# Kernel optimization log

Measured on AMD Instinct MI355X. Metric: run time of the kernel, lower is better.

The kernel has to match this reference:

```python
import jax, jax.numpy as jnp
import numpy as np

TAU = 1.0


def setup_inputs() -> dict:
    key = jax.random.key(0)
    k1, k2 = jax.random.split(key)
    z = jax.random.normal(k1, (131072, 64), dtype=jnp.float32)
    cluster_centers = jax.random.normal(k2, (512, 64), dtype=jnp.float32)
    return {"z": z, "cluster_centers": cluster_centers}


def reference(z, cluster_centers):
    # ||z - c||^2 = ||z||^2 + ||c||^2 - 2 z.c  (avoids the [B,K,D] broadcast tensor)
    z_sq = jnp.sum(z * z, axis=1, keepdims=True)              # [B, 1]
    c_sq = jnp.sum(cluster_centers * cluster_centers, axis=1)  # [K]
    cross = jnp.einsum('bd,kd->bk', z, cluster_centers)        # [B, K]
    dist_sq = z_sq + c_sq[None, :] - 2.0 * cross               # [B, K]
    q = jax.nn.softmax(-dist_sq / TAU, axis=1)                 # [B, K]
    loss = jnp.mean(jnp.sum(q * dist_sq, axis=1))
    return (q, loss)
```

## Files before the change

### kernel.cpp

```cpp
#include <hip/hip_runtime.h>

typedef short bf16x8 __attribute__((ext_vector_type(8)));
typedef float f32x4 __attribute__((ext_vector_type(4)));

#define K_CLUSTERS 512
#define DIM 64

__device__ __forceinline__ unsigned short f32_to_bf16_rne(float f) {
    unsigned int u = __float_as_uint(f);
    u += 0x7fffu + ((u >> 16) & 1u);
    return (unsigned short)(u >> 16);
}
__device__ __forceinline__ float bf16_bits_to_f32(unsigned short h) {
    return __uint_as_float(((unsigned int)h) << 16);
}

__global__ void prep_centers(const float* __restrict__ c,
                             short* __restrict__ c_hi, short* __restrict__ c_lo,
                             float* __restrict__ c_sq) {
    int idx = blockIdx.x * 256 + threadIdx.x;
    float v = c[idx];
    unsigned short h = f32_to_bf16_rne(v);
    float hf = bf16_bits_to_f32(h);
    unsigned short l = f32_to_bf16_rne(v - hf);
    c_hi[idx] = (short)h;
    c_lo[idx] = (short)l;
    float s = v * v;
    #pragma unroll
    for (int off = 1; off < 64; off <<= 1) s += __shfl_xor(s, off, 64);
    if ((threadIdx.x & 63) == 0) c_sq[idx >> 6] = s;
}

__global__ __launch_bounds__(256, 2)
void cluster_kernel(const float* __restrict__ z,
                    const short* __restrict__ c_hi,
                    const short* __restrict__ c_lo,
                    const float* __restrict__ c_sq,
                    float* __restrict__ q_out,
                    float* __restrict__ partials) {
    __shared__ __align__(16) short a_hi_s[16][72];
    __shared__ __align__(16) short a_lo_s[16][72];
    __shared__ float zsq_s[16];
    __shared__ float dist_s[16][K_CLUSTERS + 4];
    __shared__ float wloss_s[4];

    const int tid  = threadIdx.x;
    const int lane = tid & 63;
    const int wave = tid >> 6;
    const int m    = lane & 15;
    const int qd   = lane >> 4;
    const long rb  = (long)blockIdx.x * 16;

    bf16x8 bh[8][2], bl[8][2];
    #pragma unroll
    for (int t = 0; t < 8; ++t) {
        const int col = wave * 128 + t * 16 + m;
        const long boff = (long)col * DIM + qd * 8;
        #pragma unroll
        for (int kg = 0; kg < 2; ++kg) {
            bh[t][kg] = *(const bf16x8*)(c_hi + boff + kg * 32);
            bl[t][kg] = *(const bf16x8*)(c_lo + boff + kg * 32);
        }
    }

    {
        float4 v = ((const float4*)(z + rb * DIM))[tid];
        const int srow = tid >> 4;
        const int scol = (tid & 15) * 4;
        float fv[4] = {v.x, v.y, v.z, v.w};
        #pragma unroll
        for (int j = 0; j < 4; ++j) {
            unsigned short h = f32_to_bf16_rne(fv[j]);
            float hf = bf16_bits_to_f32(h);
            unsigned short l = f32_to_bf16_rne(fv[j] - hf);
            a_hi_s[srow][scol + j] = (short)h;
            a_lo_s[srow][scol + j] = (short)l;
        }
        float s = fv[0]*fv[0] + fv[1]*fv[1] + fv[2]*fv[2] + fv[3]*fv[3];
        #pragma unroll
        for (int off = 1; off < 16; off <<= 1) s += __shfl_xor(s, off, 64);
        if ((tid & 15) == 0) zsq_s[srow] = s;
    }
    __syncthreads();

    bf16x8 ah[2], al[2];
    #pragma unroll
    for (int kg = 0; kg < 2; ++kg) {
        ah[kg] = *(const bf16x8*)&a_hi_s[m][kg * 32 + qd * 8];
        al[kg] = *(const bf16x8*)&a_lo_s[m][kg * 32 + qd * 8];
    }

    f32x4 acc[8];
    #pragma unroll
    for (int t = 0; t < 8; ++t) acc[t] = (f32x4){0.f, 0.f, 0.f, 0.f};
    #pragma unroll
    for (int kg = 0; kg < 2; ++kg) {
        #pragma unroll
        for (int t = 0; t < 8; ++t) {
            acc[t] = __builtin_amdgcn_mfma_f32_16x16x32_bf16(ah[kg], bh[t][kg], acc[t], 0, 0, 0);
            acc[t] = __builtin_amdgcn_mfma_f32_16x16x32_bf16(ah[kg], bl[t][kg], acc[t], 0, 0, 0);
            acc[t] = __builtin_amdgcn_mfma_f32_16x16x32_bf16(al[kg], bh[t][kg], acc[t], 0, 0, 0);
        }
    }

    #pragma unroll
    for (int t = 0; t < 8; ++t) {
        const int col = wave * 128 + t * 16 + m;
        const float csq = c_sq[col];
        #pragma unroll
        for (int r = 0; r < 4; ++r) {
            const int row = qd * 4 + r;
            dist_s[row][col] = zsq_s[row] + csq - 2.0f * acc[t][r];
        }
    }
    __syncthreads();

    float lsum = 0.0f;
    #pragma unroll
    for (int rr = 0; rr < 4; ++rr) {
        const int row = wave * 4 + rr;
        float d[8];
        #pragma unroll
        for (int j = 0; j < 8; ++j) d[j] = dist_s[row][lane + 64 * j];
        float mn = d[0];
        #pragma unroll
        for (int j = 1; j < 8; ++j) mn = fminf(mn, d[j]);
        #pragma unroll
        for (int off = 1; off < 64; off <<= 1) mn = fminf(mn, __shfl_xor(mn, off, 64));
        float e[8], s = 0.0f;
        #pragma unroll
        for (int j = 0; j < 8; ++j) { e[j] = __expf(mn - d[j]); s += e[j]; }
        #pragma unroll
        for (int off = 1; off < 64; off <<= 1) s += __shfl_xor(s, off, 64);
        const float inv = 1.0f / s;
        float rl = 0.0f;
        float* orow = q_out + (rb + row) * K_CLUSTERS;
        #pragma unroll
        for (int j = 0; j < 8; ++j) {
            const float qv = e[j] * inv;
            orow[lane + 64 * j] = qv;
            rl += qv * d[j];
        }
        #pragma unroll
        for (int off = 1; off < 64; off <<= 1) rl += __shfl_xor(rl, off, 64);
        lsum += rl;
    }
    if (lane == 0) wloss_s[wave] = lsum;
    __syncthreads();
    if (tid == 0) partials[blockIdx.x] = wloss_s[0] + wloss_s[1] + wloss_s[2] + wloss_s[3];
}

__global__ void reduce_loss(const float* __restrict__ partials, int n,
                            float* __restrict__ loss_out, float inv_b) {
    float s = 0.f;
    for (int i = threadIdx.x; i < n; i += 256) s += partials[i];
    #pragma unroll
    for (int off = 1; off < 64; off <<= 1) s += __shfl_xor(s, off, 64);
    __shared__ float ws[4];
    if ((threadIdx.x & 63) == 0) ws[threadIdx.x >> 6] = s;
    __syncthreads();
    if (threadIdx.x == 0) loss_out[0] = (ws[0] + ws[1] + ws[2] + ws[3]) * inv_b;
}

extern "C" void kernel_launch(void* const* d_in, const int* in_sizes, int n_in,
                              void* d_out, int out_size, void* d_ws, size_t ws_size,
                              hipStream_t stream) {
    const float* z = (const float*)d_in[0];
    const float* c = (const float*)d_in[1];
    const int B = in_sizes[0] / DIM;
    float* q_out = (float*)d_out;
    float* loss_out = q_out + (size_t)B * K_CLUSTERS;

    char* ws = (char*)d_ws;
    short* c_hi    = (short*)ws;
    short* c_lo    = (short*)(ws + 65536);
    float* c_sq    = (float*)(ws + 131072);
    float* partials = (float*)(ws + 133120);

    const int nblk = B / 16;
    prep_centers<<<(K_CLUSTERS * DIM) / 256, 256, 0, stream>>>(c, c_hi, c_lo, c_sq);
    cluster_kernel<<<nblk, 256, 0, stream>>>(z, c_hi, c_lo, c_sq, q_out, partials);
    reduce_loss<<<1, 256, 0, stream>>>(partials, nblk, loss_out, 1.0f / (float)B);
}
```

Baseline: 395.7 us.

## Process four row tiles per block to reuse center fragments; atomic loss reduction

```diff
diff --git a/kernel.cpp b/kernel.cpp
--- a/kernel.cpp
+++ b/kernel.cpp
@@ -5,6 +5,7 @@
 
 #define K_CLUSTERS 512
 #define DIM 64
+#define ROWS_PER_BLOCK 64
 
 __device__ __forceinline__ unsigned short f32_to_bf16_rne(float f) {
     unsigned int u = __float_as_uint(f);
@@ -31,13 +32,18 @@
     if ((threadIdx.x & 63) == 0) c_sq[idx >> 6] = s;
 }
 
+__global__ void init_loss(float* __restrict__ loss_out) {
+    if (threadIdx.x == 0) loss_out[0] = 0.0f;
+}
+
 __global__ __launch_bounds__(256, 2)
 void cluster_kernel(const float* __restrict__ z,
                     const short* __restrict__ c_hi,
                     const short* __restrict__ c_lo,
                     const float* __restrict__ c_sq,
                     float* __restrict__ q_out,
-                    float* __restrict__ partials) {
+                    float* __restrict__ loss_out,
+                    float inv_b) {
     __shared__ __align__(16) short a_hi_s[16][72];
     __shared__ __align__(16) short a_lo_s[16][72];
     __shared__ float zsq_s[16];
@@ -49,9 +55,10 @@
     const int wave = tid >> 6;
     const int m    = lane & 15;
     const int qd   = lane >> 4;
-    const long rb  = (long)blockIdx.x * 16;
+    const long rb  = (long)blockIdx.x * ROWS_PER_BLOCK;
 
     bf16x8 bh[8][2], bl[8][2];
+    float csq[8];
     #pragma unroll
     for (int t = 0; t < 8; ++t) {
         const int col = wave * 128 + t * 16 + m;
@@ -61,105 +68,104 @@
             bh[t][kg] = *(const bf16x8*)(c_hi + boff + kg * 32);
             bl[t][kg] = *(const bf16x8*)(c_lo + boff + kg * 32);
         }
+        csq[t] = c_sq[col];
     }
 
-    {
-        float4 v = ((const float4*)(z + rb * DIM))[tid];
-        const int srow = tid >> 4;
-        const int scol = (tid & 15) * 4;
-        float fv[4] = {v.x, v.y, v.z, v.w};
+    float4 v = ((const float4*)(z + rb * DIM))[tid];
+    float lsum = 0.0f;
+
+    for (int s = 0; s < ROWS_PER_BLOCK / 16; ++s) {
+        float4 vn;
+        if (s + 1 < ROWS_PER_BLOCK / 16)
+            vn = ((const float4*)(z + (rb + (s + 1) * 16) * DIM))[tid];
+
+        {
+            const int srow = tid >> 4;
+            const int scol = (tid & 15) * 4;
+            float fv[4] = {v.x, v.y, v.z, v.w};
+            #pragma unroll
+            for (int j = 0; j < 4; ++j) {
+                unsigned short h = f32_to_bf16_rne(fv[j]);
+                float hf = bf16_bits_to_f32(h);
+                unsigned short l = f32_to_bf16_rne(fv[j] - hf);
+                a_hi_s[srow][scol + j] = (short)h;
+                a_lo_s[srow][scol + j] = (short)l;
+            }
+            float ssq = fv[0]*fv[0] + fv[1]*fv[1] + fv[2]*fv[2] + fv[3]*fv[3];
+            #pragma unroll
+            for (int off = 1; off < 16; off <<= 1) ssq += __shfl_xor(ssq, off, 64);
+            if ((tid & 15) == 0) zsq_s[srow] = ssq;
+        }
+        __syncthreads();
+
+        bf16x8 ah[2], al[2];
         #pragma unroll
-        for (int j = 0; j < 4; ++j) {
-            unsigned short h = f32_to_bf16_rne(fv[j]);
-            float hf = bf16_bits_to_f32(h);
-            unsigned short l = f32_to_bf16_rne(fv[j] - hf);
-            a_hi_s[srow][scol + j] = (short)h;
-            a_lo_s[srow][scol + j] = (short)l;
+        for (int kg = 0; kg < 2; ++kg) {
+            ah[kg] = *(const bf16x8*)&a_hi_s[m][kg * 32 + qd * 8];
+            al[kg] = *(const bf16x8*)&a_lo_s[m][kg * 32 + qd * 8];
         }
-        float s = fv[0]*fv[0] + fv[1]*fv[1] + fv[2]*fv[2] + fv[3]*fv[3];
+
+        f32x4 acc[8];
         #pragma unroll
-        for (int off = 1; off < 16; off <<= 1) s += __shfl_xor(s, off, 64);
-        if ((tid & 15) == 0) zsq_s[srow] = s;
-    }
-    __syncthreads();
+        for (int t = 0; t < 8; ++t) acc[t] = (f32x4){0.f, 0.f, 0.f, 0.f};
+        #pragma unroll
+        for (int kg = 0; kg < 2; ++kg) {
+            #pragma unroll
+            for (int t = 0; t < 8; ++t) {
+                acc[t] = __builtin_amdgcn_mfma_f32_16x16x32_bf16(ah[kg], bh[t][kg], acc[t], 0, 0, 0);
+                acc[t] = __builtin_amdgcn_mfma_f32_16x16x32_bf16(ah[kg], bl[t][kg], acc[t], 0, 0, 0);
+                acc[t] = __builtin_amdgcn_mfma_f32_16x16x32_bf16(al[kg], bh[t][kg], acc[t], 0, 0, 0);
+            }
+        }
 
-    bf16x8 ah[2], al[2];
-    #pragma unroll
-    for (int kg = 0; kg < 2; ++kg) {
-        ah[kg] = *(const bf16x8*)&a_hi_s[m][kg * 32 + qd * 8];
-        al[kg] = *(const bf16x8*)&a_lo_s[m][kg * 32 + qd * 8];
+        #pragma unroll
+        for (int t = 0; t < 8; ++t) {
+            const int col = wave * 128 + t * 16 + m;
+            #pragma unroll
+            for (int r = 0; r < 4; ++r) {
+                const int row = qd * 4 + r;
+                dist_s[row][col] = zsq_s[row] + csq[t] - 2.0f * acc[t][r];
+            }
+        }
+        __syncthreads();
+
+        const long rbase = rb + s * 16;
+        #pragma unroll
+        for (int rr = 0; rr < 4; ++rr) {
+            const int row = wave * 4 + rr;
+            float d[8];
+            #pragma unroll
+            for (int j = 0; j < 8; ++j) d[j] = dist_s[row][lane + 64 * j];
+            float mn = d[0];
+            #pragma unroll
+            for (int j = 1; j < 8; ++j) mn = fminf(mn, d[j]);
+            #pragma unroll
+            for (int off = 1; off < 64; off <<= 1) mn = fminf(mn, __shfl_xor(mn, off, 64));
+            float e[8], ssum = 0.0f;
+            #pragma unroll
+            for (int j = 0; j < 8; ++j) { e[j] = __expf(mn - d[j]); ssum += e[j]; }
+            #pragma unroll
+            for (int off = 1; off < 64; off <<= 1) ssum += __shfl_xor(ssum, off, 64);
+            const float inv = 1.0f / ssum;
+            float rl = 0.0f;
+            float* orow = q_out + (rbase + row) * K_CLUSTERS;
+            #pragma unroll
+            for (int j = 0; j < 8; ++j) {
+                const float qv = e[j] * inv;
+                orow[lane + 64 * j] = qv;
+                rl += qv * d[j];
+            }
+            #pragma unroll
+            for (int off = 1; off < 64; off <<= 1) rl += __shfl_xor(rl, off, 64);
+            lsum += rl;
+        }
+        v = vn;
     }
 
-    f32x4 acc[8];
-    #pragma unroll
-    for (int t = 0; t < 8; ++t) acc[t] = (f32x4){0.f, 0.f, 0.f, 0.f};
-    #pragma unroll
-    for (int kg = 0; kg < 2; ++kg) {
-        #pragma unroll
-        for (int t = 0; t < 8; ++t) {
-            acc[t] = __builtin_amdgcn_mfma_f32_16x16x32_bf16(ah[kg], bh[t][kg], acc[t], 0, 0, 0);
-            acc[t] = __builtin_amdgcn_mfma_f32_16x16x32_bf16(ah[kg], bl[t][kg], acc[t], 0, 0, 0);
-            acc[t] = __builtin_amdgcn_mfma_f32_16x16x32_bf16(al[kg], bh[t][kg], acc[t], 0, 0, 0);
-        }
-    }
-
-    #pragma unroll
-    for (int t = 0; t < 8; ++t) {
-        const int col = wave * 128 + t * 16 + m;
-        const float csq = c_sq[col];
-        #pragma unroll
-        for (int r = 0; r < 4; ++r) {
-            const int row = qd * 4 + r;
-            dist_s[row][col] = zsq_s[row] + csq - 2.0f * acc[t][r];
-        }
-    }
-    __syncthreads();
-
-    float lsum = 0.0f;
-    #pragma unroll
-    for (int rr = 0; rr < 4; ++rr) {
-        const int row = wave * 4 + rr;
-        float d[8];
-        #pragma unroll
-        for (int j = 0; j < 8; ++j) d[j] = dist_s[row][lane + 64 * j];
-        float mn = d[0];
-        #pragma unroll
-        for (int j = 1; j < 8; ++j) mn = fminf(mn, d[j]);
-        #pragma unroll
-        for (int off = 1; off < 64; off <<= 1) mn = fminf(mn, __shfl_xor(mn, off, 64));
-        float e[8], s = 0.0f;
-        #pragma unroll
-        for (int j = 0; j < 8; ++j) { e[j] = __expf(mn - d[j]); s += e[j]; }
-        #pragma unroll
-        for (int off = 1; off < 64; off <<= 1) s += __shfl_xor(s, off, 64);
-        const float inv = 1.0f / s;
-        float rl = 0.0f;
-        float* orow = q_out + (rb + row) * K_CLUSTERS;
-        #pragma unroll
-        for (int j = 0; j < 8; ++j) {
-            const float qv = e[j] * inv;
-            orow[lane + 64 * j] = qv;
-            rl += qv * d[j];
-        }
-        #pragma unroll
-        for (int off = 1; off < 64; off <<= 1) rl += __shfl_xor(rl, off, 64);
-        lsum += rl;
-    }
     if (lane == 0) wloss_s[wave] = lsum;
     __syncthreads();
-    if (tid == 0) partials[blockIdx.x] = wloss_s[0] + wloss_s[1] + wloss_s[2] + wloss_s[3];
-}
-
-__global__ void reduce_loss(const float* __restrict__ partials, int n,
-                            float* __restrict__ loss_out, float inv_b) {
-    float s = 0.f;
-    for (int i = threadIdx.x; i < n; i += 256) s += partials[i];
-    #pragma unroll
-    for (int off = 1; off < 64; off <<= 1) s += __shfl_xor(s, off, 64);
-    __shared__ float ws[4];
-    if ((threadIdx.x & 63) == 0) ws[threadIdx.x >> 6] = s;
-    __syncthreads();
-    if (threadIdx.x == 0) loss_out[0] = (ws[0] + ws[1] + ws[2] + ws[3]) * inv_b;
+    if (tid == 0)
+        atomicAdd(loss_out, (wloss_s[0] + wloss_s[1] + wloss_s[2] + wloss_s[3]) * inv_b);
 }
 
 extern "C" void kernel_launch(void* const* d_in, const int* in_sizes, int n_in,
@@ -172,13 +178,12 @@
     float* loss_out = q_out + (size_t)B * K_CLUSTERS;
 
     char* ws = (char*)d_ws;
-    short* c_hi    = (short*)ws;
-    short* c_lo    = (short*)(ws + 65536);
-    float* c_sq    = (float*)(ws + 131072);
-    float* partials = (float*)(ws + 133120);
+    short* c_hi = (short*)ws;
+    short* c_lo = (short*)(ws + 65536);
+    float* c_sq = (float*)(ws + 131072);
 
-    const int nblk = B / 16;
     prep_centers<<<(K_CLUSTERS * DIM) / 256, 256, 0, stream>>>(c, c_hi, c_lo, c_sq);
-    cluster_kernel<<<nblk, 256, 0, stream>>>(z, c_hi, c_lo, c_sq, q_out, partials);
-    reduce_loss<<<1, 256, 0, stream>>>(partials, nblk, loss_out, 1.0f / (float)B);
+    init_loss<<<1, 64, 0, stream>>>(loss_out);
+    cluster_kernel<<<B / ROWS_PER_BLOCK, 256, 0, stream>>>(z, c_hi, c_lo, c_sq, q_out,
+                                                           loss_out, 1.0f / (float)B);
 }
```

Measured after the change: 343.1 us. 1.15x faster.
